# Optimization experiments

Measured on AMD Instinct MI355X. Metric: run time of the kernel, lower is better.

Reference implementation:

```python
import jax, jax.numpy as jnp
import numpy as np

NUM_FILTERS = 512
NUM_HEADS = 8
D_HEAD = NUM_FILTERS // NUM_HEADS


def setup_inputs() -> dict:
    key = jax.random.key(0)
    ks = jax.random.split(key, 11)
    B, W, H, F = 4, 48, 48, NUM_FILTERS
    s = 1.0 / np.sqrt(F)
    return {
        "query": jax.random.normal(ks[0], (B, W, H, F), jnp.float32),
        "value": jax.random.normal(ks[1], (B, W, H, F), jnp.float32),
        "keys": jax.random.normal(ks[2], (B, W, H, F), jnp.float32),
        "wq_w": jax.random.normal(ks[3], (F, F), jnp.float32) * s,
        "wq_b": jnp.zeros((F,), jnp.float32),
        "wk_w": jax.random.normal(ks[4], (F, F), jnp.float32) * s,
        "wk_b": jnp.zeros((F,), jnp.float32),
        "wv_w": jax.random.normal(ks[5], (F, F), jnp.float32) * s,
        "wv_b": jnp.zeros((F,), jnp.float32),
        "wo_w": jax.random.normal(ks[6], (F, F), jnp.float32) * s,
        "wo_b": jnp.zeros((F,), jnp.float32),
    }


def reference(query, value, keys, wq_w, wq_b, wk_w, wk_b, wv_w, wv_b, wo_w, wo_b):
    B, W, H, F = query.shape
    h, d = NUM_HEADS, D_HEAD
    # flatten spatial -> sequence, project, split heads: [B, h, S, d]
    def proj(x, w, b):
        x = x.reshape(B, -1, F) @ w + b
        return x.reshape(B, -1, h, d).transpose(0, 2, 1, 3)
    q = proj(query, wq_w, wq_b)
    k = proj(keys, wk_w, wk_b)
    v = proj(value, wv_w, wv_b)
    # scaled dot-product attention (mask=None path)
    logits = jnp.einsum('bhqd,bhkd->bhqk', q, k) / jnp.sqrt(jnp.asarray(d, q.dtype))
    attn = jax.nn.softmax(logits, axis=-1)            # [B, h, S, S]
    ctx = jnp.einsum('bhqk,bhkd->bhqd', attn, v)      # [B, h, S, d]
    ctx = ctx.transpose(0, 2, 1, 3).reshape(B, -1, F)  # [B, S, F]
    out = (ctx @ wo_w + wo_b).reshape(B, W, H, F)
    attn_weights = attn.reshape(B, h, W, H, -1)        # [B, h, W, H, S]
    return out, attn_weights
```

## Files before the change

### kernel.cpp

```cpp
#include <hip/hip_runtime.h>
#include <cstddef>

#define BB 4
#define SS 2304
#define FF 512
#define NH 8
#define DD 64
#define BSR (BB*SS)

typedef __attribute__((ext_vector_type(8))) short bf16x8;
typedef __attribute__((ext_vector_type(4))) float f32x4;
#define MFMA16(a,b,c) __builtin_amdgcn_mfma_f32_16x16x32_bf16((a),(b),(c),0,0,0)

__device__ __forceinline__ ushort f2bf_rne(float x) {
    uint u = __float_as_uint(x);
    uint r = u + 0x7fffu + ((u >> 16) & 1u);
    return (ushort)(r >> 16);
}
__device__ __forceinline__ float bfval(ushort h) {
    return __uint_as_float((uint)h << 16);
}
__device__ __forceinline__ uint cvt_pk_bf16(float a, float b) {
    uint r;
    asm("v_cvt_pk_bf16_f32 %0, %1, %2" : "=v"(r) : "v"(a), "v"(b));
    return r;
}
__device__ __forceinline__ float lo16val(uint p) { return __uint_as_float(p << 16); }
__device__ __forceinline__ float hi16val(uint p) { return __uint_as_float(p & 0xffff0000u); }

__global__ __launch_bounds__(256) void wtsplit_all(
    const float* __restrict__ w0, const float* __restrict__ w1,
    const float* __restrict__ w2, const float* __restrict__ w3,
    ushort* __restrict__ whi_all, ushort* __restrict__ wlo_all)
{
    __shared__ __align__(16) float tile[64][68];
    const int z = blockIdx.z;
    const float* w = (z == 0) ? w0 : (z == 1) ? w1 : (z == 2) ? w2 : w3;
    ushort* whi = whi_all + (size_t)z * FF * FF;
    ushort* wlo = wlo_all + (size_t)z * FF * FF;

    const int t  = threadIdx.x;
    const int kt = blockIdx.x;
    const int nt = blockIdx.y;
    {
        const int r  = t >> 2;
        const int cg = (t & 3) * 16;
        const float* src = w + (size_t)(kt * 64 + r) * FF + nt * 64 + cg;
        #pragma unroll
        for (int j = 0; j < 4; ++j)
            *(float4*)&tile[r][cg + 4 * j] = *(const float4*)(src + 4 * j);
    }
    __syncthreads();
    {
        const int n  = t >> 2;
        const int kg = (t & 3) * 16;
        uint H[8], L[8];
        #pragma unroll
        for (int j = 0; j < 8; ++j) {
            float x0 = tile[kg + 2 * j][n];
            float x1 = tile[kg + 2 * j + 1][n];
            uint hp = cvt_pk_bf16(x0, x1);
            H[j] = hp;
            L[j] = cvt_pk_bf16(x0 - lo16val(hp), x1 - hi16val(hp));
        }
        size_t off = (size_t)(nt * 64 + n) * FF + kt * 64 + kg;
        *(uint4*)(whi + off)     = make_uint4(H[0], H[1], H[2], H[3]);
        *(uint4*)(whi + off + 8) = make_uint4(H[4], H[5], H[6], H[7]);
        *(uint4*)(wlo + off)     = make_uint4(L[0], L[1], L[2], L[3]);
        *(uint4*)(wlo + off + 8) = make_uint4(L[4], L[5], L[6], L[7]);
    }
}

__global__ __launch_bounds__(256) void proj_qkv(
    const float* __restrict__ q_in, const float* __restrict__ k_in,
    const float* __restrict__ v_in, const ushort* __restrict__ whi_all,
    const ushort* __restrict__ wlo_all, const float* __restrict__ bq,
    const float* __restrict__ bk, const float* __restrict__ bv,
    ushort* __restrict__ qhi,
    ushort* __restrict__ khi, ushort* __restrict__ klo,
    ushort* __restrict__ vthi)
{
    __shared__ __align__(16) ushort TL[9216];

    const int z = blockIdx.z;
    const float* X = (z == 0) ? q_in : (z == 1) ? k_in : v_in;
    const ushort* wth = whi_all + (size_t)z * FF * FF;
    const ushort* wtl = wlo_all + (size_t)z * FF * FF;
    const float* bias = (z == 0) ? bq : (z == 1) ? bk : bv;

    const int t  = threadIdx.x, w = t >> 6, l = t & 63;
    const int ar = l & 15, kg = (l >> 4) * 8;
    const int i0 = blockIdx.x * 64, j0 = blockIdx.y * 128;
    const int arow = i0 + w * 16 + ar;

    f32x4 acc[8];
    #pragma unroll
    for (int nt = 0; nt < 8; ++nt) acc[nt] = (f32x4){0.f, 0.f, 0.f, 0.f};

    for (int kk = 0; kk < FF; kk += 32) {
        const float* xr = X + (size_t)arow * FF + kk + kg;
        float4 f0 = *(const float4*)xr;
        float4 f1 = *(const float4*)(xr + 4);
        union { uint u[4]; bf16x8 v; } ah, al;
        ah.u[0] = cvt_pk_bf16(f0.x, f0.y);
        ah.u[1] = cvt_pk_bf16(f0.z, f0.w);
        ah.u[2] = cvt_pk_bf16(f1.x, f1.y);
        ah.u[3] = cvt_pk_bf16(f1.z, f1.w);
        if (z < 2) {
            al.u[0] = cvt_pk_bf16(f0.x - lo16val(ah.u[0]), f0.y - hi16val(ah.u[0]));
            al.u[1] = cvt_pk_bf16(f0.z - lo16val(ah.u[1]), f0.w - hi16val(ah.u[1]));
            al.u[2] = cvt_pk_bf16(f1.x - lo16val(ah.u[2]), f1.y - hi16val(ah.u[2]));
            al.u[3] = cvt_pk_bf16(f1.z - lo16val(ah.u[3]), f1.w - hi16val(ah.u[3]));
        }
        #pragma unroll
        for (int nt = 0; nt < 8; ++nt) {
            const size_t wo = (size_t)(j0 + nt * 16 + ar) * FF + kk + kg;
            bf16x8 bh = *(const bf16x8*)(wth + wo);
            bf16x8 bl = *(const bf16x8*)(wtl + wo);
            acc[nt] = MFMA16(ah.v, bh, acc[nt]);
            acc[nt] = MFMA16(ah.v, bl, acc[nt]);
            if (z < 2) acc[nt] = MFMA16(al.v, bh, acc[nt]);
        }
    }

    const int bidx = i0 / SS;
    const int s0b  = i0 - bidx * SS;
    const int rowl = w * 16 + ((l >> 4) << 2);

    if (z == 2) {
        #pragma unroll
        for (int nt = 0; nt < 8; ++nt) {
            const float bb = bias[j0 + nt * 16 + ar];
            #pragma unroll
            for (int r = 0; r < 4; ++r)
                TL[(nt * 16 + ar) * 72 + rowl + r] = f2bf_rne(acc[nt][r] + bb);
        }
        __syncthreads();
        const int d = t >> 1, hf = t & 1;
        const ushort* src = &TL[d * 72 + hf * 32];
        const size_t o = (((size_t)bidx * NH + ((j0 + d) >> 6)) * DD + (d & 63)) * SS
                       + s0b + hf * 32;
        *(uint4*)(vthi + o)      = *(const uint4*)(src);
        *(uint4*)(vthi + o + 8)  = *(const uint4*)(src + 8);
        *(uint4*)(vthi + o + 16) = *(const uint4*)(src + 16);
        *(uint4*)(vthi + o + 24) = *(const uint4*)(src + 24);
    } else if (z == 0) {
        const int rowf = t >> 2, qd = t & 3;
        const int colg = j0 + qd * 32;
        const size_t o = (((size_t)bidx * NH + (colg >> 6)) * SS + s0b + rowf) * DD
                       + (colg & 63);
        #pragma unroll
        for (int nt = 0; nt < 8; ++nt) {
            const float bb = bias[j0 + nt * 16 + ar];
            #pragma unroll
            for (int r = 0; r < 4; ++r)
                TL[(rowl + r) * 136 + nt * 16 + ar] = f2bf_rne(acc[nt][r] + bb);
        }
        __syncthreads();
        const ushort* src = &TL[rowf * 136 + qd * 32];
        *(uint4*)(qhi + o)      = *(const uint4*)(src);
        *(uint4*)(qhi + o + 8)  = *(const uint4*)(src + 8);
        *(uint4*)(qhi + o + 16) = *(const uint4*)(src + 16);
        *(uint4*)(qhi + o + 24) = *(const uint4*)(src + 24);
    } else {
        const int rowf = t >> 2, qd = t & 3;
        const int colg = j0 + qd * 32;
        const size_t o = (((size_t)bidx * NH + (colg >> 6)) * SS + s0b + rowf) * DD
                       + (colg & 63);
        #pragma unroll
        for (int nt = 0; nt < 8; ++nt) {
            const float bb = bias[j0 + nt * 16 + ar];
            #pragma unroll
            for (int r = 0; r < 4; ++r)
                TL[(rowl + r) * 136 + nt * 16 + ar] = f2bf_rne(acc[nt][r] + bb);
        }
        __syncthreads();
        {
            const ushort* src = &TL[rowf * 136 + qd * 32];
            *(uint4*)(khi + o)      = *(const uint4*)(src);
            *(uint4*)(khi + o + 8)  = *(const uint4*)(src + 8);
            *(uint4*)(khi + o + 16) = *(const uint4*)(src + 16);
            *(uint4*)(khi + o + 24) = *(const uint4*)(src + 24);
        }
        __syncthreads();
        #pragma unroll
        for (int nt = 0; nt < 8; ++nt) {
            const float bb = bias[j0 + nt * 16 + ar];
            #pragma unroll
            for (int r = 0; r < 4; ++r) {
                const float val = acc[nt][r] + bb;
                const ushort hv = f2bf_rne(val);
                TL[(rowl + r) * 136 + nt * 16 + ar] = f2bf_rne(val - bfval(hv));
            }
        }
        __syncthreads();
        {
            const ushort* src = &TL[rowf * 136 + qd * 32];
            *(uint4*)(klo + o)      = *(const uint4*)(src);
            *(uint4*)(klo + o + 8)  = *(const uint4*)(src + 8);
            *(uint4*)(klo + o + 16) = *(const uint4*)(src + 16);
            *(uint4*)(klo + o + 24) = *(const uint4*)(src + 24);
        }
    }
}

__global__ __launch_bounds__(256) void proj_out(
    const float* __restrict__ X, const ushort* __restrict__ wth,
    const ushort* __restrict__ wtl, const float* __restrict__ bias,
    float* __restrict__ outf)
{
    const int t  = threadIdx.x, w = t >> 6, l = t & 63;
    const int ar = l & 15, kg = (l >> 4) * 8;
    const int i0 = blockIdx.x * 64, j0 = blockIdx.y * 128;
    const int arow = i0 + w * 16 + ar;

    f32x4 acc[8];
    #pragma unroll
    for (int nt = 0; nt < 8; ++nt) acc[nt] = (f32x4){0.f, 0.f, 0.f, 0.f};

    for (int kk = 0; kk < FF; kk += 32) {
        const float* xr = X + (size_t)arow * FF + kk + kg;
        float4 f0 = *(const float4*)xr;
        float4 f1 = *(const float4*)(xr + 4);
        union { uint u[4]; bf16x8 v; } ah;
        ah.u[0] = cvt_pk_bf16(f0.x, f0.y);
        ah.u[1] = cvt_pk_bf16(f0.z, f0.w);
        ah.u[2] = cvt_pk_bf16(f1.x, f1.y);
        ah.u[3] = cvt_pk_bf16(f1.z, f1.w);
        #pragma unroll
        for (int nt = 0; nt < 8; ++nt) {
            const size_t wo = (size_t)(j0 + nt * 16 + ar) * FF + kk + kg;
            bf16x8 bh = *(const bf16x8*)(wth + wo);
            bf16x8 bl = *(const bf16x8*)(wtl + wo);
            acc[nt] = MFMA16(ah.v, bh, acc[nt]);
            acc[nt] = MFMA16(ah.v, bl, acc[nt]);
        }
    }

    #pragma unroll
    for (int nt = 0; nt < 8; ++nt) {
        const int col = j0 + nt * 16 + ar;
        const float bb = bias[col];
        #pragma unroll
        for (int r = 0; r < 4; ++r) {
            const int rowl = w * 16 + (l >> 4) * 4 + r;
            outf[(size_t)(i0 + rowl) * FF + col] = acc[nt][r] + bb;
        }
    }
}

__global__ __launch_bounds__(512, 4) void fattn_kernel(
    const ushort* __restrict__ qhi,
    const ushort* __restrict__ khi, const ushort* __restrict__ klo,
    const ushort* __restrict__ vthi,
    float* __restrict__ attn_out, float* __restrict__ ctx)
{
    __shared__ __align__(16) unsigned char smem[67584];
    ushort* KH0 = (ushort*)smem;
    ushort* KH1 = KH0 + 4096;
    ushort* KL0 = KH1 + 4096;
    ushort* KL1 = KL0 + 4096;
    ushort* VH0 = KL1 + 4096;
    ushort* VH1 = VH0 + 4096;
    float*  PT  = (float*)(VH1 + 4096);
    float*  redS = PT;

    const int t = threadIdx.x, w = t >> 6, l = t & 63;
    const int ar = l & 15, kgi = l >> 4;
    const int kg = kgi * 8;
    const int qs = w & 3, kh = w >> 2;

    const int xcd = blockIdx.x & 7;
    const int pos = blockIdx.x >> 3;
    const int bh  = xcd * 4 + (pos / 36);
    const int qt  = pos % 36;
    const int q0  = qt * 64;
    const int b   = bh >> 3, h = bh & 7;
    const size_t base = (size_t)bh * SS * DD;
    const float SC = 0.125f * 1.44269504f;

    const size_t qo = base + (size_t)(q0 + qs * 16 + ar) * DD + kg;
    const bf16x8 qh0 = *(const bf16x8*)(qhi + qo);
    const bf16x8 qh1 = *(const bf16x8*)(qhi + qo + 32);

    const int srow = t >> 3, sc8 = t & 7;
    const int sidx = srow * 64 + ((sc8 ^ (srow & 7)) << 3);
    const ushort* khsrc = khi + base + srow * 64 + sc8 * 8;
    const ushort* klsrc = klo + base + srow * 64 + sc8 * 8;
    const ushort* vhsrc = vthi + ((size_t)bh * DD + srow) * SS + sc8 * 8;

    const int sw  = ar & 7;
    const int i00 = kh * 2048 + ar * 64;
    const int i01 = i00 + 1024;
    const int s00 = (kgi ^ sw) << 3;
    const int s01 = ((4 | kgi) ^ sw) << 3;
    const int svw = ((kh * 4 + kgi) ^ sw) << 3;

    float s_[4] = {0.f, 0.f, 0.f, 0.f};
    {
        uint4 rk = *(const uint4*)khsrc;
        *(uint4*)&KH0[sidx] = rk;
        __syncthreads();
        for (int kt = 0; kt < 36; ++kt) {
            if (kt < 35) rk = *(const uint4*)(khsrc + (size_t)(kt + 1) * 4096);
            const ushort* KC = (kt & 1) ? KH1 : KH0;
            bf16x8 b00 = *(const bf16x8*)&KC[i00 + s00];
            bf16x8 b01 = *(const bf16x8*)&KC[i00 + s01];
            bf16x8 b10 = *(const bf16x8*)&KC[i01 + s00];
            bf16x8 b11 = *(const bf16x8*)&KC[i01 + s01];
            f32x4 a0 = {0.f,0.f,0.f,0.f}, a1 = {0.f,0.f,0.f,0.f};
            __builtin_amdgcn_s_setprio(1);
            a0 = MFMA16(qh0, b00, a0); a1 = MFMA16(qh0, b10, a1);
            a0 = MFMA16(qh1, b01, a0); a1 = MFMA16(qh1, b11, a1);
            __builtin_amdgcn_s_setprio(0);
            #pragma unroll
            for (int r = 0; r < 4; ++r)
                s_[r] += exp2f(a0[r] * SC) + exp2f(a1[r] * SC);
            if (kt < 35) {
                ushort* KN = (kt & 1) ? KH0 : KH1;
                *(uint4*)&KN[sidx] = rk;
            }
            __syncthreads();
        }
    }
    #pragma unroll
    for (int off = 1; off <= 8; off <<= 1) {
        #pragma unroll
        for (int r = 0; r < 4; ++r) s_[r] += __shfl_xor(s_[r], off);
    }
    if (ar == 0) {
        #pragma unroll
        for (int r = 0; r < 4; ++r)
            redS[kh * 64 + qs * 16 + kgi * 4 + r] = s_[r];
    }
    __syncthreads();
    float linv[4];
    #pragma unroll
    for (int r = 0; r < 4; ++r) {
        const int idx = qs * 16 + kgi * 4 + r;
        linv[r] = -__log2f(redS[idx] + redS[64 + idx]);
    }

    float* PTw = PT + w * 576;
    float* asto = attn_out + ((size_t)bh * SS + q0 + qs * 16 + (l >> 2)) * SS
                + kh * 32 + (l & 3) * 8;

    f32x4 acc[4];
    #pragma unroll
    for (int nt = 0; nt < 4; ++nt) acc[nt] = (f32x4){0.f, 0.f, 0.f, 0.f};

    {
        uint4 a = *(const uint4*)khsrc;
        uint4 bq = *(const uint4*)klsrc;
        uint4 c = *(const uint4*)vhsrc;
        *(uint4*)&KH0[sidx] = a;
        *(uint4*)&KL0[sidx] = bq;
        *(uint4*)&VH0[sidx] = c;
    }
    __syncthreads();

    for (int kt = 0; kt < 36; ++kt) {
        uint4 rkh, rkl, rvh;
        if (kt < 35) {
            rkh = *(const uint4*)(khsrc + (size_t)(kt + 1) * 4096);
            rkl = *(const uint4*)(klsrc + (size_t)(kt + 1) * 4096);
            rvh = *(const uint4*)(vhsrc + (size_t)(kt + 1) * 64);
        }
        const ushort* KHc = (kt & 1) ? KH1 : KH0;
        const ushort* KLc = (kt & 1) ? KL1 : KL0;
        const ushort* VHc = (kt & 1) ? VH1 : VH0;

        bf16x8 bh00 = *(const bf16x8*)&KHc[i00 + s00];
        bf16x8 bh01 = *(const bf16x8*)&KHc[i00 + s01];
        bf16x8 bl00 = *(const bf16x8*)&KLc[i00 + s00];
        bf16x8 bl01 = *(const bf16x8*)&KLc[i00 + s01];
        bf16x8 bh10 = *(const bf16x8*)&KHc[i01 + s00];
        bf16x8 bh11 = *(const bf16x8*)&KHc[i01 + s01];
        bf16x8 bl10 = *(const bf16x8*)&KLc[i01 + s00];
        bf16x8 bl11 = *(const bf16x8*)&KLc[i01 + s01];
        f32x4 a0 = {0.f,0.f,0.f,0.f}, a1 = {0.f,0.f,0.f,0.f};
        __builtin_amdgcn_s_setprio(1);
        a0 = MFMA16(qh0, bh00, a0); a1 = MFMA16(qh0, bh10, a1);
        a0 = MFMA16(qh0, bl00, a0); a1 = MFMA16(qh0, bl10, a1);
        a0 = MFMA16(qh1, bh01, a0); a1 = MFMA16(qh1, bh11, a1);
        a0 = MFMA16(qh1, bl01, a0); a1 = MFMA16(qh1, bl11, a1);
        __builtin_amdgcn_s_setprio(0);

        #pragma unroll
        for (int r = 0; r < 4; ++r) {
            const int row = kgi * 4 + r;
            float p0 = exp2f(fmaf(a0[r], SC, linv[r]));
            float p1 = exp2f(fmaf(a1[r], SC, linv[r]));
            PTw[row * 36 + ar]      = p0;
            PTw[row * 36 + 16 + ar] = p1;
        }

        {
            const float* psr = PTw + (l >> 2) * 36 + (l & 3) * 8;
            f32x4 sv0 = *(const f32x4*)psr;
            f32x4 sv1 = *(const f32x4*)(psr + 4);
            f32x4* dst = (f32x4*)(asto + (size_t)kt * 64);
            __builtin_nontemporal_store(sv0, dst);
            __builtin_nontemporal_store(sv1, dst + 1);
        }

        {
            const float* par = PTw + ar * 36 + kg;
            f32x4 pf0 = *(const f32x4*)par;
            f32x4 pf1 = *(const f32x4*)(par + 4);
            union { uint u[4]; bf16x8 v; } pah;
            pah.u[0] = cvt_pk_bf16(pf0[0], pf0[1]);
            pah.u[1] = cvt_pk_bf16(pf0[2], pf0[3]);
            pah.u[2] = cvt_pk_bf16(pf1[0], pf1[1]);
            pah.u[3] = cvt_pk_bf16(pf1[2], pf1[3]);
            __builtin_amdgcn_s_setprio(1);
            #pragma unroll
            for (int nt = 0; nt < 4; ++nt) {
                const int vfi = (nt * 16 + ar) * 64 + svw;
                bf16x8 vh = *(const bf16x8*)&VHc[vfi];
                acc[nt] = MFMA16(pah.v, vh, acc[nt]);
            }
            __builtin_amdgcn_s_setprio(0);
        }

        if (kt < 35) {
            ushort* KHN = (kt & 1) ? KH0 : KH1;
            ushort* KLN = (kt & 1) ? KL0 : KL1;
            ushort* VHN = (kt & 1) ? VH0 : VH1;
            *(uint4*)&KHN[sidx] = rkh;
            *(uint4*)&KLN[sidx] = rkl;
            *(uint4*)&VHN[sidx] = rvh;
        }
        __syncthreads();
    }

    float* SCR = (float*)smem;
    #pragma unroll
    for (int nt = 0; nt < 4; ++nt) {
        #pragma unroll
        for (int r = 0; r < 4; ++r)
            SCR[w * 1088 + (kgi * 4 + r) * 68 + nt * 16 + ar] = acc[nt][r];
    }
    __syncthreads();
    {
        const int rrow = t >> 3;
        const int dg   = (t & 7) * 8;
        const int rqs  = rrow >> 4, rl = rrow & 15;
        const float* s0p = SCR + rqs * 1088 + rl * 68 + dg;
        const float* s1p = s0p + 4 * 1088;
        f32x4 o0, o1;
        #pragma unroll
        for (int j = 0; j < 4; ++j) o0[j] = s0p[j] + s1p[j];
        #pragma unroll
        for (int j = 0; j < 4; ++j) o1[j] = s0p[4 + j] + s1p[4 + j];
        float* cdst = ctx + ((size_t)b * SS + q0 + rrow) * FF + h * DD + dg;
        *(f32x4*)cdst = o0;
        *(f32x4*)(cdst + 4) = o1;
    }
}

extern "C" void kernel_launch(void* const* d_in, const int* in_sizes, int n_in,
                              void* d_out, int out_size, void* d_ws, size_t ws_size,
                              hipStream_t stream) {
    (void)in_sizes; (void)n_in; (void)out_size; (void)ws_size;
    const float* query = (const float*)d_in[0];
    const float* value = (const float*)d_in[1];
    const float* keys  = (const float*)d_in[2];
    const float* wq_w  = (const float*)d_in[3];
    const float* wq_b  = (const float*)d_in[4];
    const float* wk_w  = (const float*)d_in[5];
    const float* wk_b  = (const float*)d_in[6];
    const float* wv_w  = (const float*)d_in[7];
    const float* wv_b  = (const float*)d_in[8];
    const float* wo_w  = (const float*)d_in[9];
    const float* wo_b  = (const float*)d_in[10];

    float* out  = (float*)d_out;
    float* attn = out + (size_t)BB * SS * FF;

    const size_t NQ = (size_t)BB * NH * SS * DD;
    ushort* qhi    = (ushort*)d_ws;
    ushort* khi    = qhi + NQ;
    ushort* klo    = khi + NQ;
    ushort* vthi   = klo + NQ;
    float*  vstage = (float*)(vthi + NQ);
    ushort* wthi   = (ushort*)(vstage + NQ);
    ushort* wtlo   = wthi + (size_t)4 * FF * FF;

    dim3 gwt(FF / 64, FF / 64, 4);
    dim3 gqkv(BSR / 64, FF / 128, 3);
    dim3 gproj(BSR / 64, FF / 128);

    wtsplit_all<<<gwt, 256, 0, stream>>>(wq_w, wk_w, wv_w, wo_w, wthi, wtlo);
    proj_qkv<<<gqkv, 256, 0, stream>>>(query, keys, value, wthi, wtlo,
                                       wq_b, wk_b, wv_b,
                                       qhi, khi, klo, vthi);

    fattn_kernel<<<36 * 32, 512, 0, stream>>>(qhi, khi, klo, vthi,
                                              attn, vstage);

    proj_out<<<gproj, 256, 0, stream>>>(vstage, wthi + (size_t)3 * FF * FF,
                                        wtlo + (size_t)3 * FF * FF, wo_b, out);
}
```

Before: 634.4 us.

## Single-buffer attention LDS tiles and XOR-swizzle probability scratch to raise occupancy

Replaces the double-buffered K-hi, K-lo and V shared-memory tiles with single buffers and adds an extra barrier before each refill. The per-wave probability scratch shrinks from a padded 36-float stride to a 32-float stride with an XOR swizzle that avoids bank conflicts. Together this cuts LDS from about 66KB to 40KB, and the launch bound is raised to 8 blocks per CU. In exchange, each iteration now has two barriers and loses the overlap of LDS writes with compute.

```diff
diff --git a/kernel.cpp b/kernel.cpp
--- a/kernel.cpp
+++ b/kernel.cpp
@@ -249,20 +249,17 @@
     }
 }
 
-__global__ __launch_bounds__(512, 4) void fattn_kernel(
+__global__ __launch_bounds__(512, 8) void fattn_kernel(
     const ushort* __restrict__ qhi,
     const ushort* __restrict__ khi, const ushort* __restrict__ klo,
     const ushort* __restrict__ vthi,
     float* __restrict__ attn_out, float* __restrict__ ctx)
 {
-    __shared__ __align__(16) unsigned char smem[67584];
-    ushort* KH0 = (ushort*)smem;
-    ushort* KH1 = KH0 + 4096;
-    ushort* KL0 = KH1 + 4096;
-    ushort* KL1 = KL0 + 4096;
-    ushort* VH0 = KL1 + 4096;
-    ushort* VH1 = VH0 + 4096;
-    float*  PT  = (float*)(VH1 + 4096);
+    __shared__ __align__(16) unsigned char smem[40960];
+    ushort* KH = (ushort*)smem;
+    ushort* KL = KH + 4096;
+    ushort* VH = KL + 4096;
+    float*  PT = (float*)(VH + 4096);
     float*  redS = PT;
 
     const int t = threadIdx.x, w = t >> 6, l = t & 63;
@@ -299,11 +296,11 @@
     float s_[4] = {0.f, 0.f, 0.f, 0.f};
     {
         uint4 rk = *(const uint4*)khsrc;
-        *(uint4*)&KH0[sidx] = rk;
+        *(uint4*)&KH[sidx] = rk;
         __syncthreads();
         for (int kt = 0; kt < 36; ++kt) {
             if (kt < 35) rk = *(const uint4*)(khsrc + (size_t)(kt + 1) * 4096);
-            const ushort* KC = (kt & 1) ? KH1 : KH0;
+            const ushort* KC = (kt & 1) ? KL : KH;
             bf16x8 b00 = *(const bf16x8*)&KC[i00 + s00];
             bf16x8 b01 = *(const bf16x8*)&KC[i00 + s01];
             bf16x8 b10 = *(const bf16x8*)&KC[i01 + s00];
@@ -317,7 +314,7 @@
             for (int r = 0; r < 4; ++r)
                 s_[r] += exp2f(a0[r] * SC) + exp2f(a1[r] * SC);
             if (kt < 35) {
-                ushort* KN = (kt & 1) ? KH0 : KH1;
+                ushort* KN = (kt & 1) ? KH : KL;
                 *(uint4*)&KN[sidx] = rk;
             }
             __syncthreads();
@@ -340,8 +337,9 @@
         const int idx = qs * 16 + kgi * 4 + r;
         linv[r] = -__log2f(redS[idx] + redS[64 + idx]);
     }
-
-    float* PTw = PT + w * 576;
+    __syncthreads();
+
+    float* PTw = PT + w * 512;
     float* asto = attn_out + ((size_t)bh * SS + q0 + qs * 16 + (l >> 2)) * SS
                 + kh * 32 + (l & 3) * 8;
 
@@ -353,12 +351,13 @@
         uint4 a = *(const uint4*)khsrc;
         uint4 bq = *(const uint4*)klsrc;
         uint4 c = *(const uint4*)vhsrc;
-        *(uint4*)&KH0[sidx] = a;
-        *(uint4*)&KL0[sidx] = bq;
-        *(uint4*)&VH0[sidx] = c;
+        *(uint4*)&KH[sidx] = a;
+        *(uint4*)&KL[sidx] = bq;
+        *(uint4*)&VH[sidx] = c;
     }
     __syncthreads();
 
+    const int ptW0a = (((ar >> 2) ^ 0) << 2) + (ar & 3);
     for (int kt = 0; kt < 36; ++kt) {
         uint4 rkh, rkl, rvh;
         if (kt < 35) {
@@ -366,18 +365,15 @@
             rkl = *(const uint4*)(klsrc + (size_t)(kt + 1) * 4096);
             rvh = *(const uint4*)(vhsrc + (size_t)(kt + 1) * 64);
         }
-        const ushort* KHc = (kt & 1) ? KH1 : KH0;
-        const ushort* KLc = (kt & 1) ? KL1 : KL0;
-        const ushort* VHc = (kt & 1) ? VH1 : VH0;
-
-        bf16x8 bh00 = *(const bf16x8*)&KHc[i00 + s00];
-        bf16x8 bh01 = *(const bf16x8*)&KHc[i00 + s01];
-        bf16x8 bl00 = *(const bf16x8*)&KLc[i00 + s00];
-        bf16x8 bl01 = *(const bf16x8*)&KLc[i00 + s01];
-        bf16x8 bh10 = *(const bf16x8*)&KHc[i01 + s00];
-        bf16x8 bh11 = *(const bf16x8*)&KHc[i01 + s01];
-        bf16x8 bl10 = *(const bf16x8*)&KLc[i01 + s00];
-        bf16x8 bl11 = *(const bf16x8*)&KLc[i01 + s01];
+
+        bf16x8 bh00 = *(const bf16x8*)&KH[i00 + s00];
+        bf16x8 bh01 = *(const bf16x8*)&KH[i00 + s01];
+        bf16x8 bl00 = *(const bf16x8*)&KL[i00 + s00];
+        bf16x8 bl01 = *(const bf16x8*)&KL[i00 + s01];
+        bf16x8 bh10 = *(const bf16x8*)&KH[i01 + s00];
+        bf16x8 bh11 = *(const bf16x8*)&KH[i01 + s01];
+        bf16x8 bl10 = *(const bf16x8*)&KL[i01 + s00];
+        bf16x8 bl11 = *(const bf16x8*)&KL[i01 + s01];
         f32x4 a0 = {0.f,0.f,0.f,0.f}, a1 = {0.f,0.f,0.f,0.f};
         __builtin_amdgcn_s_setprio(1);
         a0 = MFMA16(qh0, bh00, a0); a1 = MFMA16(qh0, bh10, a1);
@@ -389,25 +385,28 @@
         #pragma unroll
         for (int r = 0; r < 4; ++r) {
             const int row = kgi * 4 + r;
+            const int rx  = (row & 7) << 2;
             float p0 = exp2f(fmaf(a0[r], SC, linv[r]));
             float p1 = exp2f(fmaf(a1[r], SC, linv[r]));
-            PTw[row * 36 + ar]      = p0;
-            PTw[row * 36 + 16 + ar] = p1;
+            PTw[row * 32 + (ptW0a ^ rx)]        = p0;
+            PTw[row * 32 + (ptW0a ^ rx ^ 16)]   = p1;
         }
 
         {
-            const float* psr = PTw + (l >> 2) * 36 + (l & 3) * 8;
-            f32x4 sv0 = *(const f32x4*)psr;
-            f32x4 sv1 = *(const f32x4*)(psr + 4);
+            const int row = l >> 2;
+            const int rx  = (row & 7) << 2;
+            const int g0  = ((l & 3) * 2) << 2;
+            f32x4 sv0 = *(const f32x4*)&PTw[row * 32 + ((g0) ^ rx)];
+            f32x4 sv1 = *(const f32x4*)&PTw[row * 32 + ((g0 + 4) ^ rx)];
             f32x4* dst = (f32x4*)(asto + (size_t)kt * 64);
             __builtin_nontemporal_store(sv0, dst);
             __builtin_nontemporal_store(sv1, dst + 1);
         }
 
         {
-            const float* par = PTw + ar * 36 + kg;
-            f32x4 pf0 = *(const f32x4*)par;
-            f32x4 pf1 = *(const f32x4*)(par + 4);
+            const int rx = (ar & 7) << 2;
+            f32x4 pf0 = *(const f32x4*)&PTw[ar * 32 + ((kgi * 8) ^ rx)];
+            f32x4 pf1 = *(const f32x4*)&PTw[ar * 32 + ((kgi * 8 + 4) ^ rx)];
             union { uint u[4]; bf16x8 v; } pah;
             pah.u[0] = cvt_pk_bf16(pf0[0], pf0[1]);
             pah.u[1] = cvt_pk_bf16(pf0[2], pf0[3]);
@@ -417,21 +416,19 @@
             #pragma unroll
             for (int nt = 0; nt < 4; ++nt) {
                 const int vfi = (nt * 16 + ar) * 64 + svw;
-                bf16x8 vh = *(const bf16x8*)&VHc[vfi];
+                bf16x8 vh = *(const bf16x8*)&VH[vfi];
                 acc[nt] = MFMA16(pah.v, vh, acc[nt]);
             }
             __builtin_amdgcn_s_setprio(0);
         }
 
+        __syncthreads();
         if (kt < 35) {
-            ushort* KHN = (kt & 1) ? KH0 : KH1;
-            ushort* KLN = (kt & 1) ? KL0 : KL1;
-            ushort* VHN = (kt & 1) ? VH0 : VH1;
-            *(uint4*)&KHN[sidx] = rkh;
-            *(uint4*)&KLN[sidx] = rkl;
-            *(uint4*)&VHN[sidx] = rvh;
-        }
-        __syncthreads();
+            *(uint4*)&KH[sidx] = rkh;
+            *(uint4*)&KL[sidx] = rkl;
+            *(uint4*)&VH[sidx] = rvh;
+            __syncthreads();
+        }
     }
 
     float* SCR = (float*)smem;
```

New measurement: 1.161 ms. 1.83x slower.
